# Performance work log

Hardware: AMD Instinct MI355X
Metric: run time of the kernel (lower is better)

Reference implementation:

```python
import jax, jax.numpy as jnp
import numpy as np

T, N, E, F, H, LH = 24, 50000, 1_600_000, 16, 64, 128


def setup_inputs() -> dict:
    key = jax.random.key(0)
    ks = jax.random.split(key, 16)
    s = 0.1  # small init scale
    return {
        "x_seq": jax.random.normal(ks[0], (T, N, F), jnp.float32),
        "edge_index": jax.random.randint(ks[1], (2, E), 0, N, dtype=jnp.int32),
        "W1": jax.random.normal(ks[2], (F, H), jnp.float32) * s,
        "b1": jax.random.normal(ks[3], (H,), jnp.float32) * s,
        "W2": jax.random.normal(ks[4], (H, H), jnp.float32) * s,
        "b2": jax.random.normal(ks[5], (H,), jnp.float32) * s,
        "W_ih": jax.random.normal(ks[6], (4 * LH, H), jnp.float32) * s,
        "W_hh": jax.random.normal(ks[7], (4 * LH, LH), jnp.float32) * s,
        "b_ih": jax.random.normal(ks[8], (4 * LH,), jnp.float32) * s,
        "b_hh": jax.random.normal(ks[9], (4 * LH,), jnp.float32) * s,
        "Wf1": jax.random.normal(ks[10], (LH, 32), jnp.float32) * s,
        "bf1": jax.random.normal(ks[11], (32,), jnp.float32) * s,
        "Wf2": jax.random.normal(ks[12], (32, 1), jnp.float32) * s,
        "bf2": jax.random.normal(ks[13], (1,), jnp.float32) * s,
    }


def reference(x_seq, edge_index, W1, b1, W2, b2, W_ih, W_hh, b_ih, b_hh, Wf1, bf1, Wf2, bf2):
    Nn = x_seq.shape[1]
    lh = W_hh.shape[1]
    src, dst = edge_index[0], edge_index[1]

    # GCN symmetric norm with self-loops: deg counts incoming edges + self-loop
    deg = jax.ops.segment_sum(jnp.ones(src.shape[0], x_seq.dtype), dst, num_segments=Nn) + 1.0
    dinv = jax.lax.rsqrt(deg)
    enorm = dinv[src] * dinv[dst]          # (E,)
    snorm = dinv * dinv                    # (N,) self-loop norm

    def agg(xw):  # xw: (N, H')  -> D^-1/2 (A+I) D^-1/2 xw
        out = jax.ops.segment_sum(xw[src] * enorm[:, None], dst, num_segments=Nn)
        return out + xw * snorm[:, None]

    def gcn_step(_, x_t):  # x_t: (N, F)
        h = jax.nn.relu(agg(x_t @ W1) + b1)
        h = jax.nn.relu(agg(h @ W2) + b2)
        return None, h

    _, h_seq = jax.lax.scan(gcn_step, None, x_seq)  # (T, N, H)

    # single-layer LSTM (torch gate order i, f, g, o); only final h needed
    def lstm_step(carry, x_t):
        h, c = carry
        g = x_t @ W_ih.T + b_ih + h @ W_hh.T + b_hh
        i, f, gg, o = jnp.split(g, 4, axis=-1)
        c = jax.nn.sigmoid(f) * c + jax.nn.sigmoid(i) * jnp.tanh(gg)
        h = jax.nn.sigmoid(o) * jnp.tanh(c)
        return (h, c), None

    h0 = jnp.zeros((Nn, lh), x_seq.dtype)
    (hT, _), _ = jax.lax.scan(lstm_step, (h0, h0), h_seq)

    z = jax.nn.relu(hT @ Wf1 + bf1)
    return (z @ Wf2 + bf2)[:, 0]  # (N,)
```

## Files before the change

kernel.cpp:

```cpp
#include <hip/hip_runtime.h>
#include <hip/hip_bf16.h>
#include <math.h>


typedef short s16x8 __attribute__((ext_vector_type(8)));
typedef float f32x16 __attribute__((ext_vector_type(16)));
typedef unsigned long long u64;
typedef unsigned short u16;
union AF { s16x8 v; u64 q[2]; uint4 u4; };

__device__ __forceinline__ float sigf(float x) { return 1.f / (1.f + __expf(-x)); }
__device__ __forceinline__ float tanhfast(float x) { return 1.f - 2.f / (1.f + __expf(2.f * x)); }

__device__ __forceinline__ unsigned bfr(float x) {
    union { float f; unsigned u; } c; c.f = x;
    return (c.u + 0x7fffu + ((c.u >> 16) & 1u)) >> 16;
}
__device__ __forceinline__ void bsplit(float x, u16& hi, u16& lo) {
    unsigned h = bfr(x);
    union { unsigned u; float f; } hf; hf.u = h << 16;
    hi = (u16)h;
    lo = (u16)bfr(x - hf.f);
}
__device__ __forceinline__ float bf2f(u16 b) {
    union { unsigned u; float f; } c; c.u = ((unsigned)b) << 16;
    return c.f;
}

__global__ void k_count(const int* __restrict__ dst, int E, int* __restrict__ deg) {
    int e = blockIdx.x * blockDim.x + threadIdx.x;
    if (e < E) atomicAdd(&deg[dst[e]], 1);
}

__global__ void k_dinv(const int* __restrict__ deg, float* __restrict__ dinv, int N) {
    int v = blockIdx.x * blockDim.x + threadIdx.x;
    if (v < N) dinv[v] = rsqrtf((float)deg[v] + 1.0f);
}

__global__ __launch_bounds__(256) void k_scan_part(const int* __restrict__ deg, int* __restrict__ partial, int N) {
    int tid = threadIdx.x;
    int i = blockIdx.x * 256 + tid;
    int v = (i < N) ? deg[i] : 0;
    int s = v;
#pragma unroll
    for (int off = 1; off < 64; off <<= 1) s += __shfl_xor(s, off, 64);
    __shared__ int ws[4];
    if ((tid & 63) == 0) ws[tid >> 6] = s;
    __syncthreads();
    if (tid == 0) partial[blockIdx.x] = ws[0] + ws[1] + ws[2] + ws[3];
}

__global__ __launch_bounds__(256) void k_scan_top(int* __restrict__ partial, int nb) {
    __shared__ int sm[256];
    int t = threadIdx.x;
    int x = (t < nb) ? partial[t] : 0;
    sm[t] = x;
    __syncthreads();
#pragma unroll
    for (int off = 1; off < 256; off <<= 1) {
        int y = (t >= off) ? sm[t - off] : 0;
        __syncthreads();
        sm[t] += y;
        __syncthreads();
    }
    if (t < nb) partial[t] = sm[t] - x;
}

__global__ __launch_bounds__(256) void k_scan_fill(const int* __restrict__ deg, const int* __restrict__ partial,
                                                   int* __restrict__ row_ptr, int* __restrict__ cursor, int N) {
    int tid = threadIdx.x;
    int lane = tid & 63;
    int wv = tid >> 6;
    int i = blockIdx.x * 256 + tid;
    int v = (i < N) ? deg[i] : 0;
    int incl = v;
#pragma unroll
    for (int off = 1; off < 64; off <<= 1) {
        int y = __shfl_up(incl, off, 64);
        if (lane >= off) incl += y;
    }
    __shared__ int ws[4];
    if (lane == 63) ws[wv] = incl;
    __syncthreads();
    int woff = 0;
    for (int w = 0; w < wv; ++w) woff += ws[w];
    int excl = incl - v + woff + partial[blockIdx.x];
    if (i < N) {
        row_ptr[i] = excl;
        cursor[i] = excl;
        if (i == N - 1) row_ptr[N] = excl + v;
    }
}

__global__ void k_fill_range(const int* __restrict__ src, const int* __restrict__ dst, int E,
                             int* __restrict__ cursor, int* __restrict__ col, int lo, int hi) {
    int e = blockIdx.x * blockDim.x + threadIdx.x;
    if (e < E) {
        int d = dst[e];
        if (d >= lo && d < hi) {
            int p = atomicAdd(&cursor[d], 1);
            col[p] = src[e];
        }
    }
}

__global__ void k_wprep(const float* __restrict__ W_ih, const float* __restrict__ W_hh,
                        u16* __restrict__ whi, u16* __restrict__ wlo) {
    int i = blockIdx.x * 256 + threadIdx.x;
    if (i >= 512 * 192) return;
    int g = i / 192, k = i - g * 192;
    float wv = (k < 64) ? W_ih[g * 64 + k] : W_hh[g * 128 + (k - 64)];
    u16 h, l;
    bsplit(wv, h, l);
    whi[i] = h;
    wlo[i] = l;
}

__global__ void k_w2prep(const float* __restrict__ W2,
                         u16* __restrict__ w2thi, u16* __restrict__ w2tlo) {
    int i = blockIdx.x * 256 + threadIdx.x;
    if (i >= 64 * 64) return;
    int c = i >> 6, k = i & 63;
    u16 h, l;
    bsplit(W2[k * 64 + c], h, l);
    w2thi[c * 64 + k] = h;
    w2tlo[c * 64 + k] = l;
}

__global__ __launch_bounds__(256) void k_gcn1(const float* __restrict__ x, const float* __restrict__ dinv,
                                              const int* __restrict__ row_ptr, const int* __restrict__ col,
                                              const float* __restrict__ W1, const float* __restrict__ b1,
                                              u16* __restrict__ h1bf, int N) {
    __shared__ float w[16 * 64];
    __shared__ float uu[4][16];
    int tid = threadIdx.x;
    ((float4*)w)[tid] = ((const float4*)W1)[tid];
    __syncthreads();
    int lane = tid & 63;
    int wv = tid >> 6;
    int v = blockIdx.x * 4 + wv;
    if (v >= N) return;
    int cg = lane & 7;
    int eg = lane >> 3;
    int b = row_ptr[v];
    int e = row_ptr[v + 1];
    float s0 = 0.f, s1 = 0.f;
#pragma unroll 2
    for (int i = b + eg; i < e; i += 8) {
        int c = col[i];
        float2 xv = *(const float2*)(x + (size_t)c * 16 + 2 * cg);
        float dc = dinv[c];
        s0 = fmaf(dc, xv.x, s0);
        s1 = fmaf(dc, xv.y, s1);
    }
    s0 += __shfl_xor(s0, 8, 64);  s1 += __shfl_xor(s1, 8, 64);
    s0 += __shfl_xor(s0, 16, 64); s1 += __shfl_xor(s1, 16, 64);
    s0 += __shfl_xor(s0, 32, 64); s1 += __shfl_xor(s1, 32, 64);
    float dv = dinv[v];
    if (eg == 0) {
        float2 xv = *(const float2*)(x + (size_t)v * 16 + 2 * cg);
        uu[wv][2 * cg]     = dv * fmaf(dv, xv.x, s0);
        uu[wv][2 * cg + 1] = dv * fmaf(dv, xv.y, s1);
    }
    float a = b1[lane];
#pragma unroll
    for (int k = 0; k < 16; ++k)
        a = fmaf(uu[wv][k], w[k * 64 + lane], a);
    float r1 = fmaxf(a, 0.f) * dv;
    h1bf[(size_t)v * 64 + lane] = (u16)bfr(r1);
}

__global__ __launch_bounds__(256) void k_agg64p(const u16* __restrict__ h1bf,
                                                const float* __restrict__ dinv,
                                                const int* __restrict__ row_ptr, const int* __restrict__ col,
                                                u16* __restrict__ vhi, u16* __restrict__ vlo, int N) {
    int lane = threadIdx.x & 63;
    int v = blockIdx.x * 4 + (threadIdx.x >> 6);
    if (v >= N) return;
    int cp = lane & 15;
    int eg = lane >> 4;
    int b = row_ptr[v];
    int e = row_ptr[v + 1];
    float s0 = 0.f, s1 = 0.f, s2 = 0.f, s3 = 0.f;
    const uint2* tbl = (const uint2*)h1bf;
#pragma unroll 2
    for (int i = b + eg; i < e; i += 4) {
        int c = col[i];
        uint2 pw = tbl[(size_t)c * 16 + cp];
        s0 += bf2f((u16)(pw.x & 0xffffu));
        s1 += bf2f((u16)(pw.x >> 16));
        s2 += bf2f((u16)(pw.y & 0xffffu));
        s3 += bf2f((u16)(pw.y >> 16));
    }
    s0 += __shfl_xor(s0, 16, 64); s1 += __shfl_xor(s1, 16, 64);
    s2 += __shfl_xor(s2, 16, 64); s3 += __shfl_xor(s3, 16, 64);
    s0 += __shfl_xor(s0, 32, 64); s1 += __shfl_xor(s1, 32, 64);
    s2 += __shfl_xor(s2, 32, 64); s3 += __shfl_xor(s3, 32, 64);
    if (eg == 0) {
        uint2 sw = tbl[(size_t)v * 16 + cp];
        float dv = dinv[v];
        float t0 = dv * (s0 + bf2f((u16)(sw.x & 0xffffu)));
        float t1 = dv * (s1 + bf2f((u16)(sw.x >> 16)));
        float t2 = dv * (s2 + bf2f((u16)(sw.y & 0xffffu)));
        float t3 = dv * (s3 + bf2f((u16)(sw.y >> 16)));
        u16 h0, l0, h1v, l1v, h2v, l2v, h3, l3;
        bsplit(t0, h0, l0); bsplit(t1, h1v, l1v);
        bsplit(t2, h2v, l2v); bsplit(t3, h3, l3);
        uint2 oh, ol;
        oh.x = (unsigned)h0 | ((unsigned)h1v << 16);
        oh.y = (unsigned)h2v | ((unsigned)h3 << 16);
        ol.x = (unsigned)l0 | ((unsigned)l1v << 16);
        ol.y = (unsigned)l2v | ((unsigned)l3 << 16);
        *(uint2*)(vhi + (size_t)v * 64 + 4 * cp) = oh;
        *(uint2*)(vlo + (size_t)v * 64 + 4 * cp) = ol;
    }
}

__global__ __launch_bounds__(256, 2) void k_h2lstm(const u16* __restrict__ vhi, const u16* __restrict__ vlo,
                                                   const u16* __restrict__ w2thi, const u16* __restrict__ w2tlo,
                                                   const float* __restrict__ b2,
                                                   u16* __restrict__ hhi, u16* __restrict__ hlo,
                                                   float* __restrict__ cbuf,
                                                   const u16* __restrict__ whi, const u16* __restrict__ wlo,
                                                   const float* __restrict__ b_ih, const float* __restrict__ b_hh,
                                                   int N) {
    __shared__ __align__(16) char lds_hi[64 * 392];
    __shared__ __align__(16) char lds_lo[64 * 392];
    int tid = threadIdx.x;
    int lane = tid & 63;
    int w = tid >> 6;
    int row0 = blockIdx.x * 64;
    int l31 = lane & 31;
    int hf = lane >> 5;
    int col_j = w * 32 + l31;

    float cc[2][16];
#pragma unroll
    for (int s = 0; s < 2; ++s)
#pragma unroll
        for (int r = 0; r < 16; ++r) {
            int rl = (r & 3) + 8 * (r >> 2) + 4 * hf;
            int row = row0 + s * 32 + rl;
            cc[s][r] = (row < N) ? cbuf[(size_t)row * 128 + col_j] : 0.f;
        }

    for (int idx = tid; idx < 512; idx += 256) {
        int m = idx >> 3, c8 = idx & 7;
        int row = row0 + m;
        uint4 vh = make_uint4(0, 0, 0, 0), vl = make_uint4(0, 0, 0, 0);
        if (row < N) {
            vh = *(const uint4*)(vhi + (size_t)row * 64 + c8 * 8);
            vl = *(const uint4*)(vlo + (size_t)row * 64 + c8 * 8);
        }
        size_t bo = (size_t)m * 392 + 256 + (size_t)c8 * 16;
        *(uint4*)(lds_hi + bo) = vh;
        *(uint4*)(lds_lo + bo) = vl;
    }
    for (int idx = tid; idx < 512; idx += 256) {
        int m = idx >> 3, c8 = idx & 7;
        int row = row0 + m;
        uint4 vh = make_uint4(0, 0, 0, 0), vl = make_uint4(0, 0, 0, 0);
        if (row < N) {
            vh = *(const uint4*)(hhi + (size_t)row * 128 + c8 * 8);
            vl = *(const uint4*)(hlo + (size_t)row * 128 + c8 * 8);
        }
        size_t bo = (size_t)m * 392 + 128 + (size_t)c8 * 16;
        *(uint4*)(lds_hi + bo) = vh;
        *(uint4*)(lds_lo + bo) = vl;
    }
    __syncthreads();

    {
        int rowsub = w & 1, colsub = w >> 1;
        int c = colsub * 32 + l31;
        f32x16 acc;
#pragma unroll
        for (int r = 0; r < 16; ++r) acc[r] = 0.f;
        const char* ah = lds_hi + (size_t)(rowsub * 32 + l31) * 392 + 256 + (size_t)hf * 16;
        const char* al = lds_lo + (size_t)(rowsub * 32 + l31) * 392 + 256 + (size_t)hf * 16;
        const char* bh = (const char*)w2thi + (size_t)c * 128 + (size_t)hf * 16;
        const char* bl = (const char*)w2tlo + (size_t)c * 128 + (size_t)hf * 16;
#pragma unroll
        for (int kc = 0; kc < 4; ++kc) {
            AF Ahi, Alo, Bhi, Blo;
            Ahi.q[0] = *(const u64*)(ah + kc * 32); Ahi.q[1] = *(const u64*)(ah + kc * 32 + 8);
            Alo.q[0] = *(const u64*)(al + kc * 32); Alo.q[1] = *(const u64*)(al + kc * 32 + 8);
            Bhi.v = *(const s16x8*)(bh + kc * 32);
            Blo.v = *(const s16x8*)(bl + kc * 32);
            acc = __builtin_amdgcn_mfma_f32_32x32x16_bf16(Ahi.v, Bhi.v, acc, 0, 0, 0);
            acc = __builtin_amdgcn_mfma_f32_32x32x16_bf16(Alo.v, Bhi.v, acc, 0, 0, 0);
            acc = __builtin_amdgcn_mfma_f32_32x32x16_bf16(Ahi.v, Blo.v, acc, 0, 0, 0);
        }
        float bv = b2[c];
#pragma unroll
        for (int r = 0; r < 16; ++r) {
            int rl = (r & 3) + 8 * (r >> 2) + 4 * hf;
            int m = rowsub * 32 + rl;
            float val = fmaxf(acc[r] + bv, 0.f);
            u16 hh, ll;
            bsplit(val, hh, ll);
            size_t bo = (size_t)m * 392 + (size_t)c * 2;
            *(u16*)(lds_hi + bo) = hh;
            *(u16*)(lds_lo + bo) = ll;
        }
    }
    __syncthreads();

    for (int idx = tid; idx < 512; idx += 256) {
        int m = idx >> 3, c8 = idx & 7;
        int row = row0 + m;
        uint4 vh = make_uint4(0, 0, 0, 0), vl = make_uint4(0, 0, 0, 0);
        if (row < N) {
            vh = *(const uint4*)(hhi + (size_t)row * 128 + 64 + c8 * 8);
            vl = *(const uint4*)(hlo + (size_t)row * 128 + 64 + c8 * 8);
        }
        size_t bo = (size_t)m * 392 + 256 + (size_t)c8 * 16;
        *(uint4*)(lds_hi + bo) = vh;
        *(uint4*)(lds_lo + bo) = vl;
    }
    __syncthreads();

    f32x16 acc[2][4];
#pragma unroll
    for (int s = 0; s < 2; ++s)
#pragma unroll
        for (int g = 0; g < 4; ++g)
#pragma unroll
            for (int r = 0; r < 16; ++r) acc[s][g][r] = 0.f;

    const char* whc = (const char*)whi;
    const char* wlc = (const char*)wlo;
    size_t bbase[4];
#pragma unroll
    for (int g = 0; g < 4; ++g) bbase[g] = (size_t)(g * 128 + col_j) * 384 + (size_t)hf * 16;
    size_t abase0 = (size_t)l31 * 392 + (size_t)hf * 16;
    size_t abase1 = (size_t)(32 + l31) * 392 + (size_t)hf * 16;

#pragma unroll
    for (int kc = 0; kc < 12; ++kc) {
        AF ahi0, alo0, ahi1, alo1;
        size_t a0 = abase0 + (size_t)kc * 32;
        size_t a1 = abase1 + (size_t)kc * 32;
        ahi0.q[0] = *(const u64*)(lds_hi + a0); ahi0.q[1] = *(const u64*)(lds_hi + a0 + 8);
        alo0.q[0] = *(const u64*)(lds_lo + a0); alo0.q[1] = *(const u64*)(lds_lo + a0 + 8);
        ahi1.q[0] = *(const u64*)(lds_hi + a1); ahi1.q[1] = *(const u64*)(lds_hi + a1 + 8);
        alo1.q[0] = *(const u64*)(lds_lo + a1); alo1.q[1] = *(const u64*)(lds_lo + a1 + 8);
        AF bhi[4], blo[4];
#pragma unroll
        for (int g = 0; g < 4; ++g) {
            size_t bo2 = bbase[g] + (size_t)kc * 32;
            bhi[g].v = *(const s16x8*)(whc + bo2);
            blo[g].v = *(const s16x8*)(wlc + bo2);
        }
#pragma unroll
        for (int g = 0; g < 4; ++g) {
            acc[0][g] = __builtin_amdgcn_mfma_f32_32x32x16_bf16(ahi0.v, bhi[g].v, acc[0][g], 0, 0, 0);
            acc[0][g] = __builtin_amdgcn_mfma_f32_32x32x16_bf16(alo0.v, bhi[g].v, acc[0][g], 0, 0, 0);
            acc[0][g] = __builtin_amdgcn_mfma_f32_32x32x16_bf16(ahi0.v, blo[g].v, acc[0][g], 0, 0, 0);
            acc[1][g] = __builtin_amdgcn_mfma_f32_32x32x16_bf16(ahi1.v, bhi[g].v, acc[1][g], 0, 0, 0);
            acc[1][g] = __builtin_amdgcn_mfma_f32_32x32x16_bf16(alo1.v, bhi[g].v, acc[1][g], 0, 0, 0);
            acc[1][g] = __builtin_amdgcn_mfma_f32_32x32x16_bf16(ahi1.v, blo[g].v, acc[1][g], 0, 0, 0);
        }
    }

    float bi = b_ih[col_j] + b_hh[col_j];
    float bff = b_ih[128 + col_j] + b_hh[128 + col_j];
    float bg = b_ih[256 + col_j] + b_hh[256 + col_j];
    float bo = b_ih[384 + col_j] + b_hh[384 + col_j];
#pragma unroll
    for (int s = 0; s < 2; ++s) {
#pragma unroll
        for (int r = 0; r < 16; ++r) {
            int rl = (r & 3) + 8 * (r >> 2) + 4 * hf;
            int row = row0 + s * 32 + rl;
            if (row < N) {
                size_t off = (size_t)row * 128 + col_j;
                float iv = sigf(acc[s][0][r] + bi);
                float fv = sigf(acc[s][1][r] + bff);
                float gv = tanhfast(acc[s][2][r] + bg);
                float ov = sigf(acc[s][3][r] + bo);
                float cnew = fmaf(fv, cc[s][r], iv * gv);
                float hnew = ov * tanhfast(cnew);
                cbuf[off] = cnew;
                u16 hh, hl;
                bsplit(hnew, hh, hl);
                hhi[off] = hh;
                hlo[off] = hl;
            }
        }
    }
}

__global__ __launch_bounds__(256) void k_mlp(const u16* __restrict__ hhi, const u16* __restrict__ hlo,
                                             const float* __restrict__ Wf1, const float* __restrict__ bf1,
                                             const float* __restrict__ Wf2, const float* __restrict__ bf2,
                                             float* __restrict__ out, int N) {
    int lane = threadIdx.x & 63;
    int v = blockIdx.x * 4 + (threadIdx.x >> 6);
    if (v >= N) return;
    int j = lane & 31;
    int half = lane >> 5;
    const u16* hh = hhi + (size_t)v * 128 + half * 64;
    const u16* hl = hlo + (size_t)v * 128 + half * 64;
    float s = 0.f;
#pragma unroll
    for (int k = 0; k < 64; ++k) {
        float hv = bf2f(hh[k]) + bf2f(hl[k]);
        s = fmaf(hv, Wf1[(half * 64 + k) * 32 + j], s);
    }
    s += __shfl_down(s, 32, 64);
    float z = fmaxf(s + bf1[j], 0.f);
    float p = z * Wf2[j];
#pragma unroll
    for (int off = 16; off > 0; off >>= 1) p += __shfl_down(p, off, 64);
    if (lane == 0) out[v] = p + bf2[0];
}

extern "C" void kernel_launch(void* const* d_in, const int* in_sizes, int n_in,
                              void* d_out, int out_size, void* d_ws, size_t ws_size,
                              hipStream_t stream) {
    const float* x_seq = (const float*)d_in[0];
    const int* eidx = (const int*)d_in[1];
    const float* W1 = (const float*)d_in[2];
    const float* b1 = (const float*)d_in[3];
    const float* W2 = (const float*)d_in[4];
    const float* b2 = (const float*)d_in[5];
    const float* W_ih = (const float*)d_in[6];
    const float* W_hh = (const float*)d_in[7];
    const float* b_ih = (const float*)d_in[8];
    const float* b_hh = (const float*)d_in[9];
    const float* Wf1 = (const float*)d_in[10];
    const float* bf1 = (const float*)d_in[11];
    const float* Wf2 = (const float*)d_in[12];
    const float* bf2 = (const float*)d_in[13];

    int N = out_size;
    int E = in_sizes[1] / 2;
    int T = in_sizes[0] / (N * 16);
    const int* srcp = eidx;
    const int* dstp = eidx + E;

    char* ws = (char*)d_ws;
    size_t off = 0;
    auto alloc = [&](size_t bytes) -> char* {
        char* p = ws + off;
        off = (off + bytes + 255) & ~(size_t)255;
        return p;
    };
    int* deg = (int*)alloc((size_t)N * 4);
    int* row_ptr = (int*)alloc(((size_t)N + 1) * 4);
    int* cursor = (int*)alloc((size_t)N * 4);
    int* col = (int*)alloc((size_t)E * 4);
    int* partial = (int*)alloc(260 * 4);
    float* dinv = (float*)alloc((size_t)N * 4);
    u16* h1bf = (u16*)alloc((size_t)N * 64 * 2);
    u16* vhi = (u16*)alloc((size_t)N * 64 * 2);
    u16* vlo = (u16*)alloc((size_t)N * 64 * 2);
    u16* hhi = (u16*)alloc((size_t)N * 128 * 2);
    u16* hlo = (u16*)alloc((size_t)N * 128 * 2);
    float* cbuf = (float*)alloc((size_t)N * 128 * 4);
    u16* whi = (u16*)alloc((size_t)512 * 192 * 2);
    u16* wlo = (u16*)alloc((size_t)512 * 192 * 2);
    u16* w2thi = (u16*)alloc((size_t)64 * 64 * 2);
    u16* w2tlo = (u16*)alloc((size_t)64 * 64 * 2);

    hipMemsetAsync(deg, 0, (size_t)N * 4, stream);
    hipMemsetAsync(hhi, 0, (size_t)N * 128 * 2, stream);
    hipMemsetAsync(hlo, 0, (size_t)N * 128 * 2, stream);
    hipMemsetAsync(cbuf, 0, (size_t)N * 128 * 4, stream);

    int nb = (N + 255) / 256;
    k_count<<<(E + 255) / 256, 256, 0, stream>>>(dstp, E, deg);
    k_dinv<<<(N + 255) / 256, 256, 0, stream>>>(deg, dinv, N);
    k_scan_part<<<nb, 256, 0, stream>>>(deg, partial, N);
    k_scan_top<<<1, 256, 0, stream>>>(partial, nb);
    k_scan_fill<<<nb, 256, 0, stream>>>(deg, partial, row_ptr, cursor, N);
    int halfN = N / 2;
    k_fill_range<<<(E + 255) / 256, 256, 0, stream>>>(srcp, dstp, E, cursor, col, 0, halfN);
    k_fill_range<<<(E + 255) / 256, 256, 0, stream>>>(srcp, dstp, E, cursor, col, halfN, N);
    k_wprep<<<(512 * 192 + 255) / 256, 256, 0, stream>>>(W_ih, W_hh, whi, wlo);
    k_w2prep<<<(64 * 64 + 255) / 256, 256, 0, stream>>>(W2, w2thi, w2tlo);

    int node_wave_blocks = (N + 3) / 4;
    int tile_blocks = (N + 63) / 64;
    for (int t = 0; t < T; ++t) {
        const float* xt = x_seq + (size_t)t * N * 16;
        k_gcn1<<<node_wave_blocks, 256, 0, stream>>>(xt, dinv, row_ptr, col, W1, b1, h1bf, N);
        k_agg64p<<<node_wave_blocks, 256, 0, stream>>>(h1bf, dinv, row_ptr, col, vhi, vlo, N);
        k_h2lstm<<<tile_blocks, 256, 0, stream>>>(vhi, vlo, w2thi, w2tlo, b2, hhi, hlo, cbuf,
                                                  whi, wlo, b_ih, b_hh, N);
    }
    k_mlp<<<node_wave_blocks, 256, 0, stream>>>(hhi, hlo, Wf1, bf1, Wf2, bf2, (float*)d_out, N);
}
```

Baseline: 3.951 ms.

## Move second GCN linear layer from LSTM kernel into aggregation kernel

```diff
diff --git a/kernel.cpp b/kernel.cpp
--- a/kernel.cpp
+++ b/kernel.cpp
@@ -114,17 +114,6 @@
     bsplit(wv, h, l);
     whi[i] = h;
     wlo[i] = l;
-}
-
-__global__ void k_w2prep(const float* __restrict__ W2,
-                         u16* __restrict__ w2thi, u16* __restrict__ w2tlo) {
-    int i = blockIdx.x * 256 + threadIdx.x;
-    if (i >= 64 * 64) return;
-    int c = i >> 6, k = i & 63;
-    u16 h, l;
-    bsplit(W2[k * 64 + c], h, l);
-    w2thi[c * 64 + k] = h;
-    w2tlo[c * 64 + k] = l;
 }
 
 __global__ __launch_bounds__(256) void k_gcn1(const float* __restrict__ x, const float* __restrict__ dinv,
@@ -170,12 +159,21 @@
     h1bf[(size_t)v * 64 + lane] = (u16)bfr(r1);
 }
 
-__global__ __launch_bounds__(256) void k_agg64p(const u16* __restrict__ h1bf,
-                                                const float* __restrict__ dinv,
-                                                const int* __restrict__ row_ptr, const int* __restrict__ col,
-                                                u16* __restrict__ vhi, u16* __restrict__ vlo, int N) {
-    int lane = threadIdx.x & 63;
-    int v = blockIdx.x * 4 + (threadIdx.x >> 6);
+__global__ __launch_bounds__(256) void k_agg64h2(const u16* __restrict__ h1bf,
+                                                 const float* __restrict__ dinv,
+                                                 const int* __restrict__ row_ptr, const int* __restrict__ col,
+                                                 const float* __restrict__ W2, const float* __restrict__ b2,
+                                                 u16* __restrict__ h2hi, u16* __restrict__ h2lo, int N) {
+    __shared__ float w2s[64 * 64];
+    __shared__ float vv[4][64];
+    int tid = threadIdx.x;
+#pragma unroll
+    for (int i = 0; i < 4; ++i)
+        ((float4*)w2s)[tid + 256 * i] = ((const float4*)W2)[tid + 256 * i];
+    __syncthreads();
+    int lane = tid & 63;
+    int wv = tid >> 6;
+    int v = blockIdx.x * 4 + wv;
     if (v >= N) return;
     int cp = lane & 15;
     int eg = lane >> 4;
@@ -199,31 +197,30 @@
     if (eg == 0) {
         uint2 sw = tbl[(size_t)v * 16 + cp];
         float dv = dinv[v];
-        float t0 = dv * (s0 + bf2f((u16)(sw.x & 0xffffu)));
-        float t1 = dv * (s1 + bf2f((u16)(sw.x >> 16)));
-        float t2 = dv * (s2 + bf2f((u16)(sw.y & 0xffffu)));
-        float t3 = dv * (s3 + bf2f((u16)(sw.y >> 16)));
-        u16 h0, l0, h1v, l1v, h2v, l2v, h3, l3;
-        bsplit(t0, h0, l0); bsplit(t1, h1v, l1v);
-        bsplit(t2, h2v, l2v); bsplit(t3, h3, l3);
-        uint2 oh, ol;
-        oh.x = (unsigned)h0 | ((unsigned)h1v << 16);
-        oh.y = (unsigned)h2v | ((unsigned)h3 << 16);
-        ol.x = (unsigned)l0 | ((unsigned)l1v << 16);
-        ol.y = (unsigned)l2v | ((unsigned)l3 << 16);
-        *(uint2*)(vhi + (size_t)v * 64 + 4 * cp) = oh;
-        *(uint2*)(vlo + (size_t)v * 64 + 4 * cp) = ol;
-    }
-}
-
-__global__ __launch_bounds__(256, 2) void k_h2lstm(const u16* __restrict__ vhi, const u16* __restrict__ vlo,
-                                                   const u16* __restrict__ w2thi, const u16* __restrict__ w2tlo,
-                                                   const float* __restrict__ b2,
-                                                   u16* __restrict__ hhi, u16* __restrict__ hlo,
-                                                   float* __restrict__ cbuf,
-                                                   const u16* __restrict__ whi, const u16* __restrict__ wlo,
-                                                   const float* __restrict__ b_ih, const float* __restrict__ b_hh,
-                                                   int N) {
+        float4 t;
+        t.x = dv * (s0 + bf2f((u16)(sw.x & 0xffffu)));
+        t.y = dv * (s1 + bf2f((u16)(sw.x >> 16)));
+        t.z = dv * (s2 + bf2f((u16)(sw.y & 0xffffu)));
+        t.w = dv * (s3 + bf2f((u16)(sw.y >> 16)));
+        *(float4*)&vv[wv][4 * cp] = t;
+    }
+    float a = b2[lane];
+#pragma unroll
+    for (int k = 0; k < 64; ++k)
+        a = fmaf(vv[wv][k], w2s[k * 64 + lane], a);
+    float h2v = fmaxf(a, 0.f);
+    u16 hh, ll;
+    bsplit(h2v, hh, ll);
+    h2hi[(size_t)v * 64 + lane] = hh;
+    h2lo[(size_t)v * 64 + lane] = ll;
+}
+
+__global__ __launch_bounds__(256, 2) void k_lstm(const u16* __restrict__ h2hi, const u16* __restrict__ h2lo,
+                                                 u16* __restrict__ hhi, u16* __restrict__ hlo,
+                                                 float* __restrict__ cbuf,
+                                                 const u16* __restrict__ whi, const u16* __restrict__ wlo,
+                                                 const float* __restrict__ b_ih, const float* __restrict__ b_hh,
+                                                 int N) {
     __shared__ __align__(16) char lds_hi[64 * 392];
     __shared__ __align__(16) char lds_lo[64 * 392];
     int tid = threadIdx.x;
@@ -249,72 +246,22 @@
         int row = row0 + m;
         uint4 vh = make_uint4(0, 0, 0, 0), vl = make_uint4(0, 0, 0, 0);
         if (row < N) {
-            vh = *(const uint4*)(vhi + (size_t)row * 64 + c8 * 8);
-            vl = *(const uint4*)(vlo + (size_t)row * 64 + c8 * 8);
-        }
-        size_t bo = (size_t)m * 392 + 256 + (size_t)c8 * 16;
+            vh = *(const uint4*)(h2hi + (size_t)row * 64 + c8 * 8);
+            vl = *(const uint4*)(h2lo + (size_t)row * 64 + c8 * 8);
+        }
+        size_t bo = (size_t)m * 392 + (size_t)c8 * 16;
         *(uint4*)(lds_hi + bo) = vh;
         *(uint4*)(lds_lo + bo) = vl;
     }
-    for (int idx = tid; idx < 512; idx += 256) {
-        int m = idx >> 3, c8 = idx & 7;
+    for (int idx = tid; idx < 1024; idx += 256) {
+        int m = idx >> 4, c16 = idx & 15;
         int row = row0 + m;
         uint4 vh = make_uint4(0, 0, 0, 0), vl = make_uint4(0, 0, 0, 0);
         if (row < N) {
-            vh = *(const uint4*)(hhi + (size_t)row * 128 + c8 * 8);
-            vl = *(const uint4*)(hlo + (size_t)row * 128 + c8 * 8);
-        }
-        size_t bo = (size_t)m * 392 + 128 + (size_t)c8 * 16;
-        *(uint4*)(lds_hi + bo) = vh;
-        *(uint4*)(lds_lo + bo) = vl;
-    }
-    __syncthreads();
-
-    {
-        int rowsub = w & 1, colsub = w >> 1;
-        int c = colsub * 32 + l31;
-        f32x16 acc;
-#pragma unroll
-        for (int r = 0; r < 16; ++r) acc[r] = 0.f;
-        const char* ah = lds_hi + (size_t)(rowsub * 32 + l31) * 392 + 256 + (size_t)hf * 16;
-        const char* al = lds_lo + (size_t)(rowsub * 32 + l31) * 392 + 256 + (size_t)hf * 16;
-        const char* bh = (const char*)w2thi + (size_t)c * 128 + (size_t)hf * 16;
-        const char* bl = (const char*)w2tlo + (size_t)c * 128 + (size_t)hf * 16;
-#pragma unroll
-        for (int kc = 0; kc < 4; ++kc) {
-            AF Ahi, Alo, Bhi, Blo;
-            Ahi.q[0] = *(const u64*)(ah + kc * 32); Ahi.q[1] = *(const u64*)(ah + kc * 32 + 8);
-            Alo.q[0] = *(const u64*)(al + kc * 32); Alo.q[1] = *(const u64*)(al + kc * 32 + 8);
-            Bhi.v = *(const s16x8*)(bh + kc * 32);
-            Blo.v = *(const s16x8*)(bl + kc * 32);
-            acc = __builtin_amdgcn_mfma_f32_32x32x16_bf16(Ahi.v, Bhi.v, acc, 0, 0, 0);
-            acc = __builtin_amdgcn_mfma_f32_32x32x16_bf16(Alo.v, Bhi.v, acc, 0, 0, 0);
-            acc = __builtin_amdgcn_mfma_f32_32x32x16_bf16(Ahi.v, Blo.v, acc, 0, 0, 0);
-        }
-        float bv = b2[c];
-#pragma unroll
-        for (int r = 0; r < 16; ++r) {
-            int rl = (r & 3) + 8 * (r >> 2) + 4 * hf;
-            int m = rowsub * 32 + rl;
-            float val = fmaxf(acc[r] + bv, 0.f);
-            u16 hh, ll;
-            bsplit(val, hh, ll);
-            size_t bo = (size_t)m * 392 + (size_t)c * 2;
-            *(u16*)(lds_hi + bo) = hh;
-            *(u16*)(lds_lo + bo) = ll;
-        }
-    }
-    __syncthreads();
-
-    for (int idx = tid; idx < 512; idx += 256) {
-        int m = idx >> 3, c8 = idx & 7;
-        int row = row0 + m;
-        uint4 vh = make_uint4(0, 0, 0, 0), vl = make_uint4(0, 0, 0, 0);
-        if (row < N) {
-            vh = *(const uint4*)(hhi + (size_t)row * 128 + 64 + c8 * 8);
-            vl = *(const uint4*)(hlo + (size_t)row * 128 + 64 + c8 * 8);
-        }
-        size_t bo = (size_t)m * 392 + 256 + (size_t)c8 * 16;
+            vh = *(const uint4*)(hhi + (size_t)row * 128 + c16 * 8);
+            vl = *(const uint4*)(hlo + (size_t)row * 128 + c16 * 8);
+        }
+        size_t bo = (size_t)m * 392 + 128 + (size_t)c16 * 16;
         *(uint4*)(lds_hi + bo) = vh;
         *(uint4*)(lds_lo + bo) = vl;
     }
@@ -454,15 +401,13 @@
     int* partial = (int*)alloc(260 * 4);
     float* dinv = (float*)alloc((size_t)N * 4);
     u16* h1bf = (u16*)alloc((size_t)N * 64 * 2);
-    u16* vhi = (u16*)alloc((size_t)N * 64 * 2);
-    u16* vlo = (u16*)alloc((size_t)N * 64 * 2);
+    u16* h2hi = (u16*)alloc((size_t)N * 64 * 2);
+    u16* h2lo = (u16*)alloc((size_t)N * 64 * 2);
     u16* hhi = (u16*)alloc((size_t)N * 128 * 2);
     u16* hlo = (u16*)alloc((size_t)N * 128 * 2);
     float* cbuf = (float*)alloc((size_t)N * 128 * 4);
     u16* whi = (u16*)alloc((size_t)512 * 192 * 2);
     u16* wlo = (u16*)alloc((size_t)512 * 192 * 2);
-    u16* w2thi = (u16*)alloc((size_t)64 * 64 * 2);
-    u16* w2tlo = (u16*)alloc((size_t)64 * 64 * 2);
 
     hipMemsetAsync(deg, 0, (size_t)N * 4, stream);
     hipMemsetAsync(hhi, 0, (size_t)N * 128 * 2, stream);
@@ -479,16 +424,14 @@
     k_fill_range<<<(E + 255) / 256, 256, 0, stream>>>(srcp, dstp, E, cursor, col, 0, halfN);
     k_fill_range<<<(E + 255) / 256, 256, 0, stream>>>(srcp, dstp, E, cursor, col, halfN, N);
     k_wprep<<<(512 * 192 + 255) / 256, 256, 0, stream>>>(W_ih, W_hh, whi, wlo);
-    k_w2prep<<<(64 * 64 + 255) / 256, 256, 0, stream>>>(W2, w2thi, w2tlo);
 
     int node_wave_blocks = (N + 3) / 4;
-    int tile_blocks = (N + 63) / 64;
+    int lstm_blocks = (N + 63) / 64;
     for (int t = 0; t < T; ++t) {
         const float* xt = x_seq + (size_t)t * N * 16;
         k_gcn1<<<node_wave_blocks, 256, 0, stream>>>(xt, dinv, row_ptr, col, W1, b1, h1bf, N);
-        k_agg64p<<<node_wave_blocks, 256, 0, stream>>>(h1bf, dinv, row_ptr, col, vhi, vlo, N);
-        k_h2lstm<<<tile_blocks, 256, 0, stream>>>(vhi, vlo, w2thi, w2tlo, b2, hhi, hlo, cbuf,
-                                                  whi, wlo, b_ih, b_hh, N);
+        k_agg64h2<<<node_wave_blocks, 256, 0, stream>>>(h1bf, dinv, row_ptr, col, W2, b2, h2hi, h2lo, N);
+        k_lstm<<<lstm_blocks, 256, 0, stream>>>(h2hi, h2lo, hhi, hlo, cbuf, whi, wlo, b_ih, b_hh, N);
     }
     k_mlp<<<node_wave_blocks, 256, 0, stream>>>(hhi, hlo, Wf1, bf1, Wf2, bf2, (float*)d_out, N);
 }
```

Result: slower. 4.146 ms (+4.9%).
